# Kernel tuning notes

Hardware: AMD Instinct MI355X
Metric: run time of the kernel (lower is better)

The kernel has to match this reference:

```python
import jax, jax.numpy as jnp
import numpy as np

N, E, D, H, OUT, L, G = 50000, 800000, 128, 128, 128, 5, 512
EMB = L * H  # 640
BN_EPS = 1e-5


def setup_inputs() -> dict:
    key = jax.random.key(0)
    ks = jax.random.split(key, 24)
    s_h = 1.0 / np.sqrt(H)
    s_e = 1.0 / np.sqrt(EMB)
    inp = {
        'x': jax.random.normal(ks[0], (N, D), jnp.float32),
        'edge_index': jax.random.randint(ks[1], (2, E), 0, N, jnp.int32),
        'batch': jnp.sort(jax.random.randint(ks[2], (N,), 0, G, jnp.int32)),
        # per-layer GINConv MLP: Linear(D/H->H), BN(H), ReLU, Linear(H->H). D==H so stackable.
        'conv_W1': jax.random.normal(ks[3], (L, H, H), jnp.float32) * s_h,
        'conv_b1': jnp.zeros((L, H), jnp.float32),
        'conv_g1': jnp.ones((L, H), jnp.float32),
        'conv_be1': jnp.zeros((L, H), jnp.float32),
        'conv_W2': jax.random.normal(ks[4], (L, H, H), jnp.float32) * s_h,
        'conv_b2': jnp.zeros((L, H), jnp.float32),
        'eps': jnp.zeros((L,), jnp.float32),  # train_eps=True, init 0.0
        # outer BatchNorm per layer
        'bn_g': jnp.ones((L, H), jnp.float32),
        'bn_b': jnp.zeros((L, H), jnp.float32),
        # per-layer prediction heads Linear(H -> OUT)
        'pred_W': jax.random.normal(ks[5], (L, H, OUT), jnp.float32) * s_h,
        'pred_b': jnp.zeros((L, OUT), jnp.float32),
        # global_d FF(EMB): 3 stacked Linear(EMB,EMB) + shortcut
        'gW': jax.random.normal(ks[6], (3, EMB, EMB), jnp.float32) * s_e,
        'gb': jnp.zeros((3, EMB), jnp.float32),
        'gsW': jax.random.normal(ks[7], (EMB, EMB), jnp.float32) * s_e,
        'gsb': jnp.zeros((EMB,), jnp.float32),
        # local_d FF(EMB)
        'lW': jax.random.normal(ks[8], (3, EMB, EMB), jnp.float32) * s_e,
        'lb': jnp.zeros((3, EMB), jnp.float32),
        'lsW': jax.random.normal(ks[9], (EMB, EMB), jnp.float32) * s_e,
        'lsb': jnp.zeros((EMB,), jnp.float32),
    }
    return inp


def _bn(h, g, b):
    # BatchNorm1d, training mode: batch stats over node dim (biased var)
    m = jnp.mean(h, axis=0)
    v = jnp.var(h, axis=0)
    return g * (h - m) * jax.lax.rsqrt(v + BN_EPS) + b


def _ff(x, W, b, Ws, bs):
    h = x
    for i in range(3):
        h = jax.nn.relu(h @ W[i] + b[i])
    return h + x @ Ws + bs


def reference(x, edge_index, batch, conv_W1, conv_b1, conv_g1, conv_be1,
              conv_W2, conv_b2, eps, bn_g, bn_b, pred_W, pred_b,
              gW, gb, gsW, gsb, lW, lb, lsW, lsb):
    src, dst = edge_index[0], edge_index[1]
    h = x
    xs = []
    for i in range(L):
        # GINConv: (1+eps)*x_i + sum_{j->i} x_j, then MLP
        agg = jax.ops.segment_sum(h[src], dst, num_segments=N)
        h = (1.0 + eps[i]) * h + agg
        h = _bn(h @ conv_W1[i] + conv_b1[i], conv_g1[i], conv_be1[i])
        h = jax.nn.relu(h)
        h = h @ conv_W2[i] + conv_b2[i]
        h = jax.nn.relu(_bn(h, bn_g[i], bn_b[i]))
        xs.append(h)
    # per-layer graph sum-pool + prediction head (dropout in eval = identity)
    xpool = [jax.ops.segment_sum(xs[i], batch, num_segments=G) @ pred_W[i] + pred_b[i]
             for i in range(L)]
    xcat = jnp.concatenate(xpool, axis=1)            # [G, L*OUT]
    graph_embedding = _ff(xcat, gW, gb, gsW, gsb)     # [G, EMB]
    node_embedding = _ff(jnp.concatenate(xs, axis=1), lW, lb, lsW, lsb)  # [N, EMB]
    return (graph_embedding, node_embedding, xcat)
```

## Files before the change

kernel.cpp:

```cpp
#include <hip/hip_runtime.h>

constexpr int H    = 128;
constexpr int LNUM = 5;
constexpr int NG   = 512;
constexpr int EMB  = 640;
constexpr float BN_EPS = 1e-5f;

typedef __attribute__((ext_vector_type(8))) short bf16x8;
typedef __attribute__((ext_vector_type(4))) float f32x4;

__device__ inline unsigned short f2bf(float f){
  unsigned u = __builtin_bit_cast(unsigned, f);
  u += 0x7FFF + ((u >> 16) & 1);
  return (unsigned short)(u >> 16);
}
__device__ inline float bf2f(unsigned short h){
  unsigned u = ((unsigned)h) << 16;
  return __builtin_bit_cast(float, u);
}

__device__ inline int xcd_swz(int bid, int nwg){
  int q = nwg >> 3, r = nwg & 7;
  int xcd = bid & 7, idx = bid >> 3;
  return (xcd < r ? xcd*(q+1) : r*(q+1) + (xcd-r)*q) + idx;
}

__global__ void k_zerof(float* p, int n){
  int i = blockIdx.x*256 + threadIdx.x;
  if (i < n) p[i] = 0.f;
}
__global__ void k_zeroi(int* p, int n){
  int i = blockIdx.x*256 + threadIdx.x;
  if (i < n) p[i] = 0;
}

__global__ void k_hist(const int* __restrict__ dst, int E, int* deg){
  int e = blockIdx.x*256 + threadIdx.x;
  if (e < E) atomicAdd(&deg[dst[e]], 1);
}

__global__ __launch_bounds__(1024) void k_scan(int* degcur, int* __restrict__ rowptr, int n){
  __shared__ int wsum[16];
  __shared__ int carry;
  int tid = threadIdx.x, wid = tid >> 6, lane = tid & 63;
  if (tid == 0){ carry = 0; rowptr[0] = 0; }
  __syncthreads();
  for (int base = 0; base < n; base += 1024){
    int v = (base + tid < n) ? degcur[base + tid] : 0;
    int s = v;
#pragma unroll
    for (int off = 1; off < 64; off <<= 1){
      int t = __shfl_up(s, off);
      if (lane >= off) s += t;
    }
    if (lane == 63) wsum[wid] = s;
    __syncthreads();
    if (wid == 0 && lane < 16){
      int wv = wsum[lane];
#pragma unroll
      for (int off = 1; off < 16; off <<= 1){
        int t = __shfl_up(wv, off);
        if (lane >= off) wv += t;
      }
      wsum[lane] = wv;
    }
    __syncthreads();
    int incl = s + (wid ? wsum[wid-1] : 0) + carry;
    if (base + tid < n){ rowptr[base + tid + 1] = incl; degcur[base + tid] = incl - v; }
    __syncthreads();
    if (tid == 0) carry += wsum[15];
    __syncthreads();
  }
}

__global__ void k_scatter(const int* __restrict__ src, const int* __restrict__ dst,
                          int E, int* cursor, int* __restrict__ colsrc){
  int e = blockIdx.x*256 + threadIdx.x;
  if (e < E){
    int d = dst[e];
    int pos = atomicAdd(&cursor[d], 1);
    colsrc[pos] = src[e];
  }
}

__global__ void k_gstart(const int* __restrict__ batch, int N, int* __restrict__ gstart){
  int g = blockIdx.x*256 + threadIdx.x;
  if (g <= NG){
    int lo = 0, hi = N;
    while (lo < hi){
      int mid = (lo + hi) >> 1;
      if (batch[mid] < g) lo = mid + 1; else hi = mid;
    }
    gstart[g] = lo;
  }
}

__global__ void k_castT(const float* __restrict__ W, unsigned short* __restrict__ Wt,
                        int K, int Nn, int ldt, int koff){
  __shared__ float sh[32][33];
  const size_t in_off  = (size_t)blockIdx.z * K * Nn;
  const size_t out_off = (size_t)blockIdx.z * Nn * ldt;
  int n0 = blockIdx.x*32, k0 = blockIdx.y*32;
  int tx = threadIdx.x, ty = threadIdx.y;
  for (int r = ty; r < 32; r += 8)
    sh[r][tx] = W[in_off + (size_t)(k0 + r)*Nn + n0 + tx];
  __syncthreads();
  for (int r = ty; r < 32; r += 8)
    Wt[out_off + (size_t)(n0 + r)*ldt + koff + k0 + tx] = f2bf(sh[tx][r]);
}

__global__ void k_bias2(const float* __restrict__ a, const float* __restrict__ b,
                        float* __restrict__ o){
  int i = threadIdx.x;
  o[i] = a[i] + b[i];
}

__global__ __launch_bounds__(320) void k_pool(const unsigned short* __restrict__ xall,
                                              const int* __restrict__ gstart,
                                              float* __restrict__ pooled){
  int g = blockIdx.x;
  int t = threadIdx.x;
  int n0 = gstart[g], n1 = gstart[g+1];
  float a0 = 0.f, a1 = 0.f;
  for (int n = n0; n < n1; ++n){
    unsigned u = ((const unsigned*)xall)[(size_t)n*(EMB/2) + t];
    a0 += bf2f((unsigned short)u); a1 += bf2f((unsigned short)(u >> 16));
  }
  *(float2*)(pooled + (size_t)g*EMB + 2*t) = make_float2(a0, a1);
}

__global__ __launch_bounds__(128) void k_pred(const float* __restrict__ pooled,
                                              const float* __restrict__ W,
                                              const float* __restrict__ b,
                                              float* __restrict__ xcat){
  int g = blockIdx.x, l = blockIdx.y, o = threadIdx.x;
  __shared__ float sh[128];
  sh[o] = pooled[(size_t)g*EMB + l*H + o];
  __syncthreads();
  const float* Wl = W + (size_t)l*H*H;
  float acc = b[l*H + o];
  for (int k = 0; k < H; ++k) acc = fmaf(sh[k], Wl[k*H + o], acc);
  xcat[(size_t)g*EMB + l*H + o] = acc;
}

template<bool RELU, bool OUT_BF16, bool DUAL>
__global__ __launch_bounds__(512) void k_mm(
    const unsigned short* __restrict__ A, int lda,
    const unsigned short* __restrict__ A2,
    const unsigned short* __restrict__ Bt, int ldb,
    const float* __restrict__ bias,
    void* __restrict__ Cv, int ldc,
    int M, int K)
{
  __shared__ union LdsU {
    unsigned short stage[2][2][8192];
    unsigned short sc16[128*136];
    float          sc32[128*132];
  } u;
  const int tid  = threadIdx.x;
  const int lane = tid & 63;
  const int w    = tid >> 6;
  const int wr   = w >> 2, wc = w & 3;

  const int nwg = gridDim.x * gridDim.y;
  const int bid = blockIdx.y * gridDim.x + blockIdx.x;
  const int wg  = xcd_swz(bid, nwg);
  const int col0 = (wg % gridDim.x) * 128;
  const int row0 = (wg / gridDim.x) * 128;
  const int KA   = DUAL ? (K >> 1) : K;

  const unsigned short *sA[2], *sA2p[2], *sB[2];
  int dOff[2];
#pragma unroll
  for (int j = 0; j < 2; ++j){
    int d = w*2048 + j*1024 + lane*16;
    int m = d >> 7;
    int inner = (d & 127) ^ ((m & 7) << 4);
    int gm = row0 + m; if (gm > M-1) gm = M-1;
    sA[j]  = A + (size_t)gm*lda + (inner >> 1);
    if (DUAL) sA2p[j] = A2 + (size_t)gm*lda + (inner >> 1);
    sB[j]  = Bt + (size_t)(col0 + m)*ldb + (inner >> 1);
    dOff[j] = w*2048 + j*1024;
  }

  f32x4 acc[4][2];
#pragma unroll
  for (int i = 0; i < 4; ++i)
#pragma unroll
    for (int j = 0; j < 2; ++j)
      acc[i][j] = (f32x4){0.f, 0.f, 0.f, 0.f};

  auto STAGE = [&](int buf, int kt){
    int k0 = kt*64, ka = k0;
    bool second = DUAL && (k0 >= KA);
    if (second) ka = k0 - KA;
#pragma unroll
    for (int j = 0; j < 2; ++j){
      const unsigned short* s = second ? (sA2p[j] + ka) : (sA[j] + ka);
      __builtin_amdgcn_global_load_lds(
          (const __attribute__((address_space(1))) void*)s,
          (__attribute__((address_space(3))) void*)((char*)&u.stage[buf][0][0] + dOff[j]),
          16, 0, 0);
    }
#pragma unroll
    for (int j = 0; j < 2; ++j)
      __builtin_amdgcn_global_load_lds(
          (const __attribute__((address_space(1))) void*)(sB[j] + k0),
          (__attribute__((address_space(3))) void*)((char*)&u.stage[buf][1][0] + dOff[j]),
          16, 0, 0);
  };

  const int NT = K / 64;
  STAGE(0, 0);
  STAGE(1, 1);
  asm volatile("s_waitcnt vmcnt(4)" ::: "memory");
  asm volatile("s_barrier" ::: "memory");

  for (int t = 0; t < NT; ++t){
    const char* Ab = (const char*)&u.stage[t & 1][0][0];
    const char* Bb = (const char*)&u.stage[t & 1][1][0];
    bf16x8 af[2][4], bq[2][2];
#pragma unroll
    for (int kk = 0; kk < 2; ++kk){
      const int kb = kk*64 + ((lane >> 4) << 4);
#pragma unroll
      for (int i = 0; i < 4; ++i){
        int row = wr*64 + i*16 + (lane & 15);
        af[kk][i] = *(const bf16x8*)(Ab + ((row*128 + kb) ^ ((row & 7) << 4)));
      }
#pragma unroll
      for (int j = 0; j < 2; ++j){
        int col = wc*32 + j*16 + (lane & 15);
        bq[kk][j] = *(const bf16x8*)(Bb + ((col*128 + kb) ^ ((col & 7) << 4)));
      }
    }
    if (t + 2 < NT){
      asm volatile("s_barrier" ::: "memory");
      STAGE(t & 1, t + 2);
    }
#pragma unroll
    for (int kk = 0; kk < 2; ++kk)
#pragma unroll
      for (int i = 0; i < 4; ++i)
#pragma unroll
        for (int j = 0; j < 2; ++j)
          acc[i][j] = __builtin_amdgcn_mfma_f32_16x16x32_bf16(af[kk][i], bq[kk][j], acc[i][j], 0, 0, 0);
    if (t + 1 < NT){
      if (t + 2 < NT) asm volatile("s_waitcnt vmcnt(4)" ::: "memory");
      else            asm volatile("s_waitcnt vmcnt(0)" ::: "memory");
      asm volatile("s_barrier" ::: "memory");
    }
  }

  __syncthreads();
  if (OUT_BF16){
#pragma unroll
    for (int j = 0; j < 2; ++j){
      int cl = wc*32 + j*16 + (lane & 15);
      float bs = bias[col0 + cl];
#pragma unroll
      for (int i = 0; i < 4; ++i){
        int rb = wr*64 + i*16 + ((lane >> 4) << 2);
#pragma unroll
        for (int r = 0; r < 4; ++r){
          float v = acc[i][j][r] + bs;
          if (RELU) v = fmaxf(v, 0.f);
          u.sc16[(rb + r)*136 + cl] = f2bf(v);
        }
      }
    }
    __syncthreads();
    unsigned short* Cb = (unsigned short*)Cv;
    for (int idx = tid; idx < 128*16; idx += 512){
      int rr = idx >> 4, seg = idx & 15;
      int grow = row0 + rr;
      if (grow < M){
        uint4 vv = *(const uint4*)&u.sc16[rr*136 + seg*8];
        *(uint4*)(Cb + (size_t)grow*ldc + col0 + seg*8) = vv;
      }
    }
  } else {
#pragma unroll
    for (int j = 0; j < 2; ++j){
      int cl = wc*32 + j*16 + (lane & 15);
      float bs = bias[col0 + cl];
#pragma unroll
      for (int i = 0; i < 4; ++i){
        int rb = wr*64 + i*16 + ((lane >> 4) << 2);
#pragma unroll
        for (int r = 0; r < 4; ++r){
          float v = acc[i][j][r] + bs;
          if (RELU) v = fmaxf(v, 0.f);
          u.sc32[(rb + r)*132 + cl] = v;
        }
      }
    }
    __syncthreads();
    float* Cf = (float*)Cv;
    for (int idx = tid; idx < 128*32; idx += 512){
      int rr = idx >> 5, seg = idx & 31;
      int grow = row0 + rr;
      if (grow < M){
        float4 vv = *(const float4*)&u.sc32[rr*132 + seg*4];
        *(float4*)(Cf + (size_t)grow*ldc + col0 + seg*4) = vv;
      }
    }
  }
}

template<bool IN_BF16>
__global__ __launch_bounds__(512) void k_mmca(
    const void* __restrict__ hin, int ldh,
    const int* __restrict__ rowptr, const int* __restrict__ colsrc,
    const float* __restrict__ epsp,
    const unsigned short* __restrict__ Bt,
    const float* __restrict__ bias,
    unsigned short* __restrict__ C, int ldc,
    float* __restrict__ sums, float* __restrict__ sumsq,
    int M)
{
  __shared__ unsigned short shm[2*128*128];
  unsigned short* As = shm;
  unsigned short* Bs = shm + 16384;
  const int tid  = threadIdx.x;
  const int lane = tid & 63;
  const int w    = tid >> 6;
  const int wr   = w >> 2, wc = w & 3;

  const int wg   = xcd_swz(blockIdx.x, gridDim.x);
  const int row0 = wg * 128;

#pragma unroll
  for (int j = 0; j < 4; ++j){
    int d = w*4096 + j*1024 + lane*16;
    int m = d >> 8;
    int inner = (d & 255) ^ ((m & 15) << 4);
    __builtin_amdgcn_global_load_lds(
        (const __attribute__((address_space(1))) void*)(Bt + (size_t)m*H + (inner >> 1)),
        (__attribute__((address_space(3))) void*)((char*)Bs + w*4096 + j*1024),
        16, 0, 0);
  }

  {
    int r  = tid >> 2;
    int c0 = (tid & 3) << 5;
    int node = row0 + r; if (node > M-1) node = M-1;
    float ep = 1.0f + *epsp;
    float a[32];
    if (IN_BF16){
      const unsigned short* src = (const unsigned short*)hin + (size_t)node*ldh + c0;
#pragma unroll
      for (int q = 0; q < 4; ++q){
        uint2 v = *(const uint2*)(src + q*8);
        a[q*8+0] = ep*bf2f((unsigned short)v.x);  a[q*8+1] = ep*bf2f((unsigned short)(v.x>>16));
        uint2 v2 = *(const uint2*)(src + q*8 + 4);
        a[q*8+2] = ep*bf2f((unsigned short)v.y);  a[q*8+3] = ep*bf2f((unsigned short)(v.y>>16));
        a[q*8+4] = ep*bf2f((unsigned short)v2.x); a[q*8+5] = ep*bf2f((unsigned short)(v2.x>>16));
        a[q*8+6] = ep*bf2f((unsigned short)v2.y); a[q*8+7] = ep*bf2f((unsigned short)(v2.y>>16));
      }
    } else {
      const float* src = (const float*)hin + (size_t)node*ldh + c0;
#pragma unroll
      for (int q = 0; q < 32; q += 4){
        float4 f = *(const float4*)(src + q);
        a[q] = ep*f.x; a[q+1] = ep*f.y; a[q+2] = ep*f.z; a[q+3] = ep*f.w;
      }
    }
    int e = rowptr[node], e1 = rowptr[node+1];
    for (; e < e1; ++e){
      int s = colsrc[e];
      if (IN_BF16){
        const unsigned short* p = (const unsigned short*)hin + (size_t)s*ldh + c0;
        uint4 v0 = *(const uint4*)(p);
        uint4 v1 = *(const uint4*)(p + 8);
        uint4 v2 = *(const uint4*)(p + 16);
        uint4 v3 = *(const uint4*)(p + 24);
        const unsigned* uu[4] = {(const unsigned*)&v0, (const unsigned*)&v1,
                                 (const unsigned*)&v2, (const unsigned*)&v3};
#pragma unroll
        for (int q = 0; q < 4; ++q)
#pragma unroll
          for (int k = 0; k < 4; ++k){
            unsigned x = uu[q][k];
            a[q*8 + 2*k]     += bf2f((unsigned short)x);
            a[q*8 + 2*k + 1] += bf2f((unsigned short)(x >> 16));
          }
      } else {
        const float* p = (const float*)hin + (size_t)s*ldh + c0;
#pragma unroll
        for (int q = 0; q < 32; q += 4){
          float4 f = *(const float4*)(p + q);
          a[q] += f.x; a[q+1] += f.y; a[q+2] += f.z; a[q+3] += f.w;
        }
      }
    }
#pragma unroll
    for (int q = 0; q < 4; ++q){
      unsigned pk[4];
#pragma unroll
      for (int k = 0; k < 4; ++k)
        pk[k] = (unsigned)f2bf(a[q*8 + 2*k]) | ((unsigned)f2bf(a[q*8 + 2*k + 1]) << 16);
      int byte = (r*256 + (tid & 3)*64 + q*16) ^ ((r & 15) << 4);
      *(uint4*)((char*)As + byte) = *(uint4*)pk;
    }
  }

  asm volatile("s_waitcnt vmcnt(0)" ::: "memory");
  __syncthreads();

  f32x4 acc[4][2];
#pragma unroll
  for (int i = 0; i < 4; ++i)
#pragma unroll
    for (int j = 0; j < 2; ++j)
      acc[i][j] = (f32x4){0.f, 0.f, 0.f, 0.f};

#pragma unroll
  for (int kk = 0; kk < 4; ++kk){
    const int kb = kk*64 + ((lane >> 4) << 4);
    bf16x8 af[4], bfr[2];
#pragma unroll
    for (int i = 0; i < 4; ++i){
      int row = wr*64 + i*16 + (lane & 15);
      af[i] = *(const bf16x8*)((const char*)As + ((row*256 + kb) ^ ((row & 15) << 4)));
    }
#pragma unroll
    for (int j = 0; j < 2; ++j){
      int col = wc*32 + j*16 + (lane & 15);
      bfr[j] = *(const bf16x8*)((const char*)Bs + ((col*256 + kb) ^ ((col & 15) << 4)));
    }
#pragma unroll
    for (int i = 0; i < 4; ++i)
#pragma unroll
      for (int j = 0; j < 2; ++j)
        acc[i][j] = __builtin_amdgcn_mfma_f32_16x16x32_bf16(af[i], bfr[j], acc[i][j], 0, 0, 0);
  }

#pragma unroll
  for (int j = 0; j < 2; ++j){
    int col = wc*32 + j*16 + (lane & 15);
    float bs = bias[col];
    float s = 0.f, q = 0.f;
#pragma unroll
    for (int i = 0; i < 4; ++i){
      int rb = row0 + wr*64 + i*16 + ((lane >> 4) << 2);
#pragma unroll
      for (int r = 0; r < 4; ++r){
        if (rb + r < M){
          float v = acc[i][j][r] + bs;
          s += v; q += v*v;
        }
      }
    }
    s += __shfl_xor(s, 16); q += __shfl_xor(q, 16);
    s += __shfl_xor(s, 32); q += __shfl_xor(q, 32);
    if (lane < 16){
      atomicAdd(&sums[col], s);
      atomicAdd(&sumsq[col], q);
    }
  }

  __syncthreads();
#pragma unroll
  for (int j = 0; j < 2; ++j){
    int cl = wc*32 + j*16 + (lane & 15);
    float bs = bias[cl];
#pragma unroll
    for (int i = 0; i < 4; ++i){
      int rb = wr*64 + i*16 + ((lane >> 4) << 2);
#pragma unroll
      for (int r = 0; r < 4; ++r)
        shm[(rb + r)*136 + cl] = f2bf(acc[i][j][r] + bs);
    }
  }
  __syncthreads();
  for (int idx = tid; idx < 128*16; idx += 512){
    int rr = idx >> 4, seg = idx & 15;
    int grow = row0 + rr;
    if (grow < M){
      uint4 vv = *(const uint4*)&shm[rr*136 + seg*8];
      *(uint4*)(C + (size_t)grow*ldc + seg*8) = vv;
    }
  }
}

__global__ __launch_bounds__(512) void k_mmc2(
    const unsigned short* __restrict__ A,
    const unsigned short* __restrict__ Bt,
    const float* __restrict__ bias,
    const float* __restrict__ statin,
    const float* __restrict__ g1, const float* __restrict__ be1,
    float invn,
    unsigned short* __restrict__ C, int ldc,
    float* __restrict__ sums, float* __restrict__ sumsq,
    int M)
{
  __shared__ unsigned short shm[2*128*128];
  __shared__ float bnsc[128], bnsf[128];
  unsigned short* As = shm;
  unsigned short* Bs = shm + 16384;
  const int tid  = threadIdx.x;
  const int lane = tid & 63;
  const int w    = tid >> 6;
  const int wr   = w >> 2, wc = w & 3;

  const int wg   = xcd_swz(blockIdx.x, gridDim.x);
  const int row0 = wg * 128;

#pragma unroll
  for (int j = 0; j < 4; ++j){
    int d = w*4096 + j*1024 + lane*16;
    int m = d >> 8;
    int inner = (d & 255) ^ ((m & 15) << 4);
    int gm = row0 + m; if (gm > M-1) gm = M-1;
    __builtin_amdgcn_global_load_lds(
        (const __attribute__((address_space(1))) void*)(A + (size_t)gm*H + (inner >> 1)),
        (__attribute__((address_space(3))) void*)((char*)As + w*4096 + j*1024),
        16, 0, 0);
    __builtin_amdgcn_global_load_lds(
        (const __attribute__((address_space(1))) void*)(Bt + (size_t)m*H + (inner >> 1)),
        (__attribute__((address_space(3))) void*)((char*)Bs + w*4096 + j*1024),
        16, 0, 0);
  }

  if (tid < 128){
    float m = statin[tid]*invn;
    float v = statin[128 + tid]*invn - m*m;
    float inv = rsqrtf(v + BN_EPS);
    float sc = g1[tid]*inv;
    bnsc[tid] = sc;
    bnsf[tid] = be1[tid] - m*sc;
  }

  asm volatile("s_waitcnt vmcnt(0)" ::: "memory");
  __syncthreads();

  f32x4 acc[4][2];
#pragma unroll
  for (int i = 0; i < 4; ++i)
#pragma unroll
    for (int j = 0; j < 2; ++j)
      acc[i][j] = (f32x4){0.f, 0.f, 0.f, 0.f};

#pragma unroll
  for (int kk = 0; kk < 4; ++kk){
    const int kb = kk*64 + ((lane >> 4) << 4);
    bf16x8 af[4], bfr[2];
#pragma unroll
    for (int i = 0; i < 4; ++i){
      int row = wr*64 + i*16 + (lane & 15);
      af[i] = *(const bf16x8*)((const char*)As + ((row*256 + kb) ^ ((row & 15) << 4)));
    }
#pragma unroll
    for (int j = 0; j < 2; ++j){
      int col = wc*32 + j*16 + (lane & 15);
      bfr[j] = *(const bf16x8*)((const char*)Bs + ((col*256 + kb) ^ ((col & 15) << 4)));
    }
    {
      int k8 = kk*32 + ((lane >> 4) << 3);
      float4 s0 = *(const float4*)(&bnsc[k8]), s1 = *(const float4*)(&bnsc[k8 + 4]);
      float4 f0 = *(const float4*)(&bnsf[k8]), f1 = *(const float4*)(&bnsf[k8 + 4]);
      float sc[8] = {s0.x,s0.y,s0.z,s0.w,s1.x,s1.y,s1.z,s1.w};
      float sf[8] = {f0.x,f0.y,f0.z,f0.w,f1.x,f1.y,f1.z,f1.w};
#pragma unroll
      for (int i = 0; i < 4; ++i){
        bf16x8 aa = af[i], o;
#pragma unroll
        for (int jj = 0; jj < 8; ++jj){
          float v = fmaxf(fmaf(sc[jj], bf2f((unsigned short)aa[jj]), sf[jj]), 0.f);
          o[jj] = (short)f2bf(v);
        }
        af[i] = o;
      }
    }
#pragma unroll
    for (int i = 0; i < 4; ++i)
#pragma unroll
      for (int j = 0; j < 2; ++j)
        acc[i][j] = __builtin_amdgcn_mfma_f32_16x16x32_bf16(af[i], bfr[j], acc[i][j], 0, 0, 0);
  }

#pragma unroll
  for (int j = 0; j < 2; ++j){
    int col = wc*32 + j*16 + (lane & 15);
    float bs = bias[col];
    float s = 0.f, q = 0.f;
#pragma unroll
    for (int i = 0; i < 4; ++i){
      int rb = row0 + wr*64 + i*16 + ((lane >> 4) << 2);
#pragma unroll
      for (int r = 0; r < 4; ++r){
        if (rb + r < M){
          float v = acc[i][j][r] + bs;
          s += v; q += v*v;
        }
      }
    }
    s += __shfl_xor(s, 16); q += __shfl_xor(q, 16);
    s += __shfl_xor(s, 32); q += __shfl_xor(q, 32);
    if (lane < 16){
      atomicAdd(&sums[col], s);
      atomicAdd(&sumsq[col], q);
    }
  }

  __syncthreads();
#pragma unroll
  for (int j = 0; j < 2; ++j){
    int cl = wc*32 + j*16 + (lane & 15);
    float bs = bias[cl];
#pragma unroll
    for (int i = 0; i < 4; ++i){
      int rb = wr*64 + i*16 + ((lane >> 4) << 2);
#pragma unroll
      for (int r = 0; r < 4; ++r)
        shm[(rb + r)*136 + cl] = f2bf(acc[i][j][r] + bs);
    }
  }
  __syncthreads();
  for (int idx = tid; idx < 128*16; idx += 512){
    int rr = idx >> 4, seg = idx & 15;
    int grow = row0 + rr;
    if (grow < M){
      uint4 vv = *(const uint4*)&shm[rr*136 + seg*8];
      *(uint4*)(C + (size_t)grow*ldc + seg*8) = vv;
    }
  }
}

__global__ __launch_bounds__(256) void k_bnapply(const unsigned short* __restrict__ U,
                                                 const float* __restrict__ statp,
                                                 const float* __restrict__ g,
                                                 const float* __restrict__ b,
                                                 float invn,
                                                 unsigned short* __restrict__ out,
                                                 int ldo, int n){
  int i = blockIdx.x*256 + threadIdx.x;
  int total = n * (H/4);
  if (i < total){
    int r = i >> 5;
    int c4 = (i & 31) << 2;
    float4 sm = *(const float4*)(statp + c4);
    float4 sq = *(const float4*)(statp + 128 + c4);
    float4 gg = *(const float4*)(g + c4);
    float4 bb = *(const float4*)(b + c4);
    float m0 = sm.x*invn, m1 = sm.y*invn, m2 = sm.z*invn, m3 = sm.w*invn;
    float s0 = gg.x*rsqrtf(sq.x*invn - m0*m0 + BN_EPS);
    float s1 = gg.y*rsqrtf(sq.y*invn - m1*m1 + BN_EPS);
    float s2 = gg.z*rsqrtf(sq.z*invn - m2*m2 + BN_EPS);
    float s3 = gg.w*rsqrtf(sq.w*invn - m3*m3 + BN_EPS);
    float f0 = bb.x - m0*s0, f1 = bb.y - m1*s1, f2 = bb.z - m2*s2, f3 = bb.w - m3*s3;
    uint2 up = *(const uint2*)(U + (size_t)r*H + c4);
    float a = fmaxf(fmaf(s0, bf2f((unsigned short)up.x),       f0), 0.f);
    float c = fmaxf(fmaf(s1, bf2f((unsigned short)(up.x>>16)), f1), 0.f);
    float d = fmaxf(fmaf(s2, bf2f((unsigned short)up.y),       f2), 0.f);
    float e = fmaxf(fmaf(s3, bf2f((unsigned short)(up.y>>16)), f3), 0.f);
    uint2 o;
    o.x = (unsigned)f2bf(a) | ((unsigned)f2bf(c) << 16);
    o.y = (unsigned)f2bf(d) | ((unsigned)f2bf(e) << 16);
    *(uint2*)(out + (size_t)r*ldo + c4) = o;
  }
}

template<bool RELU, bool ADD_D>
__global__ __launch_bounds__(256) void k_gemm64(
    const float* __restrict__ A, int lda,
    const float* __restrict__ B, int ldb,
    const float* __restrict__ bias,
    const float* D, int ldd,
    float* C, int ldc,
    int M, int N, int K)
{
  __shared__ float As[32][68];
  __shared__ float Bs[32][64];
  const int tid  = threadIdx.x;
  const int tx   = tid & 15;
  const int ty   = tid >> 4;
  const int row0 = blockIdx.x * 64;
  const int col0 = blockIdx.y * 64;
  const int am = tid >> 3;
  const int ak = (tid & 7) << 2;
  const int bk = tid >> 4;
  const int bn = (tid & 15) << 2;
  float acc[4][4] = {};

  for (int k0 = 0; k0 < K; k0 += 32){
#pragma unroll
    for (int h = 0; h < 2; ++h){
      int m  = am + h*32;
      int gr = row0 + m;
      float4 v = make_float4(0.f, 0.f, 0.f, 0.f);
      if (gr < M) v = *(const float4*)(A + (size_t)gr*lda + k0 + ak);
      As[ak+0][m]=v.x; As[ak+1][m]=v.y; As[ak+2][m]=v.z; As[ak+3][m]=v.w;
    }
#pragma unroll
    for (int h = 0; h < 2; ++h){
      int kk = bk + h*16;
      *(float4*)(&Bs[kk][bn]) = *(const float4*)(B + (size_t)(k0+kk)*ldb + col0 + bn);
    }
    __syncthreads();
#pragma unroll 8
    for (int k = 0; k < 32; ++k){
      float4 a = *(const float4*)(&As[k][ty<<2]);
      float4 b = *(const float4*)(&Bs[k][tx<<2]);
      float av[4] = {a.x,a.y,a.z,a.w};
      float bv[4] = {b.x,b.y,b.z,b.w};
#pragma unroll
      for (int i = 0; i < 4; ++i)
#pragma unroll
        for (int j = 0; j < 4; ++j)
          acc[i][j] = fmaf(av[i], bv[j], acc[i][j]);
    }
    __syncthreads();
  }

  const int col = col0 + (tx<<2);
  float4 bv = *(const float4*)(bias + col);
#pragma unroll
  for (int i = 0; i < 4; ++i){
    int row = row0 + (ty<<2) + i;
    if (row < M){
      float r[4] = {acc[i][0]+bv.x, acc[i][1]+bv.y, acc[i][2]+bv.z, acc[i][3]+bv.w};
      if (RELU){
#pragma unroll
        for (int j = 0; j < 4; ++j) r[j] = fmaxf(r[j], 0.f);
      }
      if (ADD_D){
        float4 d = *(const float4*)(D + (size_t)row*ldd + col);
        r[0]+=d.x; r[1]+=d.y; r[2]+=d.z; r[3]+=d.w;
      }
      *(float4*)(C + (size_t)row*ldc + col) = make_float4(r[0],r[1],r[2],r[3]);
    }
  }
}

extern "C" void kernel_launch(void* const* d_in, const int* in_sizes, int n_in,
                              void* d_out, int out_size, void* d_ws, size_t ws_size,
                              hipStream_t stream) {
  const float* x        = (const float*)d_in[0];
  const int*   ei       = (const int*)d_in[1];
  const int*   batch    = (const int*)d_in[2];
  const float* conv_W1  = (const float*)d_in[3];
  const float* conv_b1  = (const float*)d_in[4];
  const float* conv_g1  = (const float*)d_in[5];
  const float* conv_be1 = (const float*)d_in[6];
  const float* conv_W2  = (const float*)d_in[7];
  const float* conv_b2  = (const float*)d_in[8];
  const float* epsv     = (const float*)d_in[9];
  const float* bn_g     = (const float*)d_in[10];
  const float* bn_b     = (const float*)d_in[11];
  const float* pred_W   = (const float*)d_in[12];
  const float* pred_b   = (const float*)d_in[13];
  const float* gW       = (const float*)d_in[14];
  const float* gb       = (const float*)d_in[15];
  const float* gsW      = (const float*)d_in[16];
  const float* gsb      = (const float*)d_in[17];
  const float* lW       = (const float*)d_in[18];
  const float* lb       = (const float*)d_in[19];
  const float* lsW      = (const float*)d_in[20];
  const float* lsb      = (const float*)d_in[21];

  const int N = in_sizes[0] / H;
  const int E = in_sizes[1] / 2;
  const int* srcI = ei;
  const int* dstI = ei + E;

  float* out = (float*)d_out;
  float* GE = out;
  float* NE = out + (size_t)NG*EMB;
  float* XC = NE + (size_t)N*EMB;

  unsigned short* xall = (unsigned short*)d_ws;
  unsigned short* h1   = xall + (size_t)N*EMB;
  unsigned short* h2   = h1 + (size_t)N*EMB;
  unsigned short* ub   = h1;
  unsigned short* tb   = h1 + (size_t)N*H;

  float* pooled  = (float*)(h2 + (size_t)N*EMB);
  float* gtmp1   = pooled + (size_t)NG*EMB;
  float* gtmp2   = gtmp1 + (size_t)NG*EMB;
  float* slots   = gtmp2 + (size_t)NG*EMB;
  float* biasNE  = slots + 2560;
  unsigned short* W1t   = (unsigned short*)(biasNE + EMB);
  unsigned short* W2t   = W1t + (size_t)LNUM*H*H;
  unsigned short* lWt01 = W2t + (size_t)LNUM*H*H;
  unsigned short* Wcat  = lWt01 + (size_t)2*EMB*EMB;
  int* rowptr = (int*)(Wcat + (size_t)2*EMB*EMB);
  int* cursor = rowptr + (N + 1);
  int* colsrc = cursor + N;
  int* gstart = colsrc + E;

  k_zerof<<<10, 256, 0, stream>>>(slots, 2560);

  k_zeroi<<<(N+255)/256, 256, 0, stream>>>(cursor, N);
  k_hist<<<(E+255)/256, 256, 0, stream>>>(dstI, E, cursor);
  k_scan<<<1, 1024, 0, stream>>>(cursor, rowptr, N);
  k_scatter<<<(E+255)/256, 256, 0, stream>>>(srcI, dstI, E, cursor, colsrc);
  k_gstart<<<(NG+256)/256, 256, 0, stream>>>(batch, N, gstart);

  const dim3 tb32(32, 8);
  k_castT<<<dim3(H/32, H/32, LNUM), tb32, 0, stream>>>(conv_W1, W1t, H, H, H, 0);
  k_castT<<<dim3(H/32, H/32, LNUM), tb32, 0, stream>>>(conv_W2, W2t, H, H, H, 0);
  k_castT<<<dim3(EMB/32, EMB/32, 2), tb32, 0, stream>>>(lW, lWt01, EMB, EMB, EMB, 0);
  k_castT<<<dim3(EMB/32, EMB/32, 1), tb32, 0, stream>>>(lW + (size_t)2*EMB*EMB, Wcat,
                                                        EMB, EMB, 2*EMB, 0);
  k_castT<<<dim3(EMB/32, EMB/32, 1), tb32, 0, stream>>>(lsW, Wcat, EMB, EMB, 2*EMB, EMB);
  k_bias2<<<1, EMB, 0, stream>>>(lb + (size_t)2*EMB, lsb, biasNE);

  const float invn = 1.0f / (float)N;
  const int nrow = (N + 127)/128;

  for (int l = 0; l < LNUM; ++l){
    float* slot1 = slots + (size_t)l*512;
    float* slot2 = slot1 + 256;

    if (l == 0)
      k_mmca<false><<<nrow, 512, 0, stream>>>(
          x, H, rowptr, colsrc, epsv, W1t, conv_b1,
          ub, H, slot1, slot1 + 128, N);
    else
      k_mmca<true><<<nrow, 512, 0, stream>>>(
          xall + (size_t)(l-1)*H, EMB, rowptr, colsrc, epsv + l,
          W1t + (size_t)l*H*H, conv_b1 + l*H,
          ub, H, slot1, slot1 + 128, N);

    k_mmc2<<<nrow, 512, 0, stream>>>(
        ub, W2t + (size_t)l*H*H, conv_b2 + l*H,
        slot1, conv_g1 + l*H, conv_be1 + l*H, invn,
        tb, H, slot2, slot2 + 128, N);

    k_bnapply<<<(N*32 + 255)/256, 256, 0, stream>>>(
        tb, slot2, bn_g + l*H, bn_b + l*H, invn,
        xall + (size_t)l*H, EMB, N);
  }

  k_pool<<<NG, 320, 0, stream>>>(xall, gstart, pooled);
  k_pred<<<dim3(NG, LNUM), 128, 0, stream>>>(pooled, pred_W, pred_b, XC);

  const dim3 gg((NG + 63)/64, EMB/64);
  k_gemm64<false,false><<<gg, 256, 0, stream>>>(XC, EMB, gsW, EMB, gsb,
                                                nullptr, 0, GE, EMB, NG, EMB, EMB);
  k_gemm64<true,false><<<gg, 256, 0, stream>>>(XC, EMB, gW, EMB, gb,
                                               nullptr, 0, gtmp1, EMB, NG, EMB, EMB);
  k_gemm64<true,false><<<gg, 256, 0, stream>>>(gtmp1, EMB, gW + (size_t)EMB*EMB, EMB, gb + EMB,
                                               nullptr, 0, gtmp2, EMB, NG, EMB, EMB);
  k_gemm64<true,true><<<gg, 256, 0, stream>>>(gtmp2, EMB, gW + (size_t)2*EMB*EMB, EMB, gb + 2*EMB,
                                              GE, EMB, GE, EMB, NG, EMB, EMB);

  const dim3 gn(EMB/128, nrow);
  k_mm<true,true,false><<<gn, 512, 0, stream>>>(
      xall, EMB, nullptr, lWt01, EMB, lb, h1, EMB, N, EMB);
  k_mm<true,true,false><<<gn, 512, 0, stream>>>(
      h1, EMB, nullptr, lWt01 + (size_t)EMB*EMB, EMB, lb + EMB, h2, EMB, N, EMB);
  k_mm<false,false,true><<<gn, 512, 0, stream>>>(
      h2, EMB, xall, Wcat, 2*EMB, biasNE, NE, EMB, N, 2*EMB);
}
```

Before: 1.074 ms.

## Replace BN atomics with per-block partials, warp-per-row gather, sorted CSR, smaller FF tiles

The batch-norm statistics are now written as per-workgroup partial sums and reduced later, which removes the global float atomics and the zeroing kernel. Neighbor aggregation gives each row to one wavefront that reads 128-channel rows in a coalesced way, two edges at a time. CSR segments are sorted by source for locality, graph pooling applies BN+ReLU from the pre-BN buffer, and the small graph FF GEMM uses 32-row tiles for more blocks. The cost is an extra insertion-sort kernel, a reduction over roughly 391 partials in every consuming block, and a serial per-wave edge loop.

```diff
diff --git a/kernel.cpp b/kernel.cpp
--- a/kernel.cpp
+++ b/kernel.cpp
@@ -25,10 +25,6 @@
   return (xcd < r ? xcd*(q+1) : r*(q+1) + (xcd-r)*q) + idx;
 }
 
-__global__ void k_zerof(float* p, int n){
-  int i = blockIdx.x*256 + threadIdx.x;
-  if (i < n) p[i] = 0.f;
-}
 __global__ void k_zeroi(int* p, int n){
   int i = blockIdx.x*256 + threadIdx.x;
   if (i < n) p[i] = 0;
@@ -80,6 +76,19 @@
     int d = dst[e];
     int pos = atomicAdd(&cursor[d], 1);
     colsrc[pos] = src[e];
+  }
+}
+
+__global__ void k_sortseg(const int* __restrict__ rowptr, int* __restrict__ colsrc, int n){
+  int node = blockIdx.x*256 + threadIdx.x;
+  if (node < n){
+    int lo = rowptr[node], hi = rowptr[node+1];
+    for (int i = lo + 1; i < hi; ++i){
+      int v = colsrc[i];
+      int j = i - 1;
+      while (j >= lo && colsrc[j] > v){ colsrc[j+1] = colsrc[j]; --j; }
+      colsrc[j+1] = v;
+    }
   }
 }
 
@@ -115,16 +124,23 @@
   o[i] = a[i] + b[i];
 }
 
-__global__ __launch_bounds__(320) void k_pool(const unsigned short* __restrict__ xall,
+__global__ __launch_bounds__(320) void k_pool(const unsigned short* __restrict__ xpre,
+                                              const float* __restrict__ bnsc2,
+                                              const float* __restrict__ bnsf2,
                                               const int* __restrict__ gstart,
                                               float* __restrict__ pooled){
   int g = blockIdx.x;
   int t = threadIdx.x;
+  int f0 = 2*t;
+  int l = f0 >> 7, c = f0 & 127;
+  float sc0 = bnsc2[l*128 + c],     sf0 = bnsf2[l*128 + c];
+  float sc1 = bnsc2[l*128 + c + 1], sf1 = bnsf2[l*128 + c + 1];
   int n0 = gstart[g], n1 = gstart[g+1];
   float a0 = 0.f, a1 = 0.f;
   for (int n = n0; n < n1; ++n){
-    unsigned u = ((const unsigned*)xall)[(size_t)n*(EMB/2) + t];
-    a0 += bf2f((unsigned short)u); a1 += bf2f((unsigned short)(u >> 16));
+    unsigned u = ((const unsigned*)xpre)[(size_t)n*(EMB/2) + t];
+    a0 += fmaxf(fmaf(sc0, bf2f((unsigned short)u),        sf0), 0.f);
+    a1 += fmaxf(fmaf(sc1, bf2f((unsigned short)(u >> 16)), sf1), 0.f);
   }
   *(float2*)(pooled + (size_t)g*EMB + 2*t) = make_float2(a0, a1);
 }
@@ -316,10 +332,11 @@
     const unsigned short* __restrict__ Bt,
     const float* __restrict__ bias,
     unsigned short* __restrict__ C, int ldc,
-    float* __restrict__ sums, float* __restrict__ sumsq,
+    float* __restrict__ pa,
     int M)
 {
   __shared__ unsigned short shm[2*128*128];
+  __shared__ float sbs[2][128], sbq[2][128];
   unsigned short* As = shm;
   unsigned short* Bs = shm + 16384;
   const int tid  = threadIdx.x;
@@ -342,66 +359,46 @@
   }
 
   {
-    int r  = tid >> 2;
-    int c0 = (tid & 3) << 5;
-    int node = row0 + r; if (node > M-1) node = M-1;
+    const int ld2 = ldh >> 1;
     float ep = 1.0f + *epsp;
-    float a[32];
-    if (IN_BF16){
-      const unsigned short* src = (const unsigned short*)hin + (size_t)node*ldh + c0;
-#pragma unroll
-      for (int q = 0; q < 4; ++q){
-        uint2 v = *(const uint2*)(src + q*8);
-        a[q*8+0] = ep*bf2f((unsigned short)v.x);  a[q*8+1] = ep*bf2f((unsigned short)(v.x>>16));
-        uint2 v2 = *(const uint2*)(src + q*8 + 4);
-        a[q*8+2] = ep*bf2f((unsigned short)v.y);  a[q*8+3] = ep*bf2f((unsigned short)(v.y>>16));
-        a[q*8+4] = ep*bf2f((unsigned short)v2.x); a[q*8+5] = ep*bf2f((unsigned short)(v2.x>>16));
-        a[q*8+6] = ep*bf2f((unsigned short)v2.y); a[q*8+7] = ep*bf2f((unsigned short)(v2.y>>16));
-      }
-    } else {
-      const float* src = (const float*)hin + (size_t)node*ldh + c0;
-#pragma unroll
-      for (int q = 0; q < 32; q += 4){
-        float4 f = *(const float4*)(src + q);
-        a[q] = ep*f.x; a[q+1] = ep*f.y; a[q+2] = ep*f.z; a[q+3] = ep*f.w;
-      }
-    }
-    int e = rowptr[node], e1 = rowptr[node+1];
-    for (; e < e1; ++e){
-      int s = colsrc[e];
+    for (int rr = 0; rr < 16; ++rr){
+      int r = w*16 + rr;
+      int node = row0 + r; if (node > M-1) node = M-1;
+      float a0, a1;
       if (IN_BF16){
-        const unsigned short* p = (const unsigned short*)hin + (size_t)s*ldh + c0;
-        uint4 v0 = *(const uint4*)(p);
-        uint4 v1 = *(const uint4*)(p + 8);
-        uint4 v2 = *(const uint4*)(p + 16);
-        uint4 v3 = *(const uint4*)(p + 24);
-        const unsigned* uu[4] = {(const unsigned*)&v0, (const unsigned*)&v1,
-                                 (const unsigned*)&v2, (const unsigned*)&v3};
-#pragma unroll
-        for (int q = 0; q < 4; ++q)
-#pragma unroll
-          for (int k = 0; k < 4; ++k){
-            unsigned x = uu[q][k];
-            a[q*8 + 2*k]     += bf2f((unsigned short)x);
-            a[q*8 + 2*k + 1] += bf2f((unsigned short)(x >> 16));
-          }
+        unsigned v = ((const unsigned*)hin)[(size_t)node*ld2 + lane];
+        a0 = ep*bf2f((unsigned short)v); a1 = ep*bf2f((unsigned short)(v >> 16));
       } else {
-        const float* p = (const float*)hin + (size_t)s*ldh + c0;
-#pragma unroll
-        for (int q = 0; q < 32; q += 4){
-          float4 f = *(const float4*)(p + q);
-          a[q] += f.x; a[q+1] += f.y; a[q+2] += f.z; a[q+3] += f.w;
+        float2 f = ((const float2*)hin)[(size_t)node*ld2 + lane];
+        a0 = ep*f.x; a1 = ep*f.y;
+      }
+      int e = rowptr[node], e1 = rowptr[node+1];
+      for (; e + 2 <= e1; e += 2){
+        int s0 = colsrc[e], s1 = colsrc[e+1];
+        if (IN_BF16){
+          unsigned v0 = ((const unsigned*)hin)[(size_t)s0*ld2 + lane];
+          unsigned v1 = ((const unsigned*)hin)[(size_t)s1*ld2 + lane];
+          a0 += bf2f((unsigned short)v0) + bf2f((unsigned short)v1);
+          a1 += bf2f((unsigned short)(v0 >> 16)) + bf2f((unsigned short)(v1 >> 16));
+        } else {
+          float2 f0 = ((const float2*)hin)[(size_t)s0*ld2 + lane];
+          float2 f1 = ((const float2*)hin)[(size_t)s1*ld2 + lane];
+          a0 += f0.x + f1.x; a1 += f0.y + f1.y;
         }
       }
-    }
-#pragma unroll
-    for (int q = 0; q < 4; ++q){
-      unsigned pk[4];
-#pragma unroll
-      for (int k = 0; k < 4; ++k)
-        pk[k] = (unsigned)f2bf(a[q*8 + 2*k]) | ((unsigned)f2bf(a[q*8 + 2*k + 1]) << 16);
-      int byte = (r*256 + (tid & 3)*64 + q*16) ^ ((r & 15) << 4);
-      *(uint4*)((char*)As + byte) = *(uint4*)pk;
+      for (; e < e1; ++e){
+        int s = colsrc[e];
+        if (IN_BF16){
+          unsigned v = ((const unsigned*)hin)[(size_t)s*ld2 + lane];
+          a0 += bf2f((unsigned short)v); a1 += bf2f((unsigned short)(v >> 16));
+        } else {
+          float2 f = ((const float2*)hin)[(size_t)s*ld2 + lane];
+          a0 += f.x; a1 += f.y;
+        }
+      }
+      unsigned pk = (unsigned)f2bf(a0) | ((unsigned)f2bf(a1) << 16);
+      int byte = (r*256 + lane*4) ^ ((r & 15) << 4);
+      *(unsigned*)((char*)As + byte) = pk;
     }
   }
 
@@ -454,10 +451,12 @@
     }
     s += __shfl_xor(s, 16); q += __shfl_xor(q, 16);
     s += __shfl_xor(s, 32); q += __shfl_xor(q, 32);
-    if (lane < 16){
-      atomicAdd(&sums[col], s);
-      atomicAdd(&sumsq[col], q);
-    }
+    if (lane < 16){ sbs[wr][col] = s; sbq[wr][col] = q; }
+  }
+  __syncthreads();
+  if (tid < 128){
+    pa[(size_t)wg*256 + tid]       = sbs[0][tid] + sbs[1][tid];
+    pa[(size_t)wg*256 + 128 + tid] = sbq[0][tid] + sbq[1][tid];
   }
 
   __syncthreads();
@@ -488,23 +487,25 @@
     const unsigned short* __restrict__ A,
     const unsigned short* __restrict__ Bt,
     const float* __restrict__ bias,
-    const float* __restrict__ statin,
+    const float* __restrict__ pa,
     const float* __restrict__ g1, const float* __restrict__ be1,
     float invn,
     unsigned short* __restrict__ C, int ldc,
-    float* __restrict__ sums, float* __restrict__ sumsq,
+    float* __restrict__ pb,
     int M)
 {
   __shared__ unsigned short shm[2*128*128];
   __shared__ float bnsc[128], bnsf[128];
+  __shared__ float rs[4][128], rq[4][128];
   unsigned short* As = shm;
   unsigned short* Bs = shm + 16384;
   const int tid  = threadIdx.x;
   const int lane = tid & 63;
   const int w    = tid >> 6;
   const int wr   = w >> 2, wc = w & 3;
-
-  const int wg   = xcd_swz(blockIdx.x, gridDim.x);
+  const int nwg  = gridDim.x;
+
+  const int wg   = xcd_swz(blockIdx.x, nwg);
   const int row0 = wg * 128;
 
 #pragma unroll
@@ -523,9 +524,21 @@
         16, 0, 0);
   }
 
+  {
+    int c = tid & 127, part = tid >> 7;
+    float s = 0.f, q = 0.f;
+    for (int bi = part; bi < nwg; bi += 4){
+      s += pa[(size_t)bi*256 + c];
+      q += pa[(size_t)bi*256 + 128 + c];
+    }
+    rs[part][c] = s; rq[part][c] = q;
+  }
+  __syncthreads();
   if (tid < 128){
-    float m = statin[tid]*invn;
-    float v = statin[128 + tid]*invn - m*m;
+    float s = rs[0][tid] + rs[1][tid] + rs[2][tid] + rs[3][tid];
+    float q = rq[0][tid] + rq[1][tid] + rq[2][tid] + rq[3][tid];
+    float m = s*invn;
+    float v = q*invn - m*m;
     float inv = rsqrtf(v + BN_EPS);
     float sc = g1[tid]*inv;
     bnsc[tid] = sc;
@@ -580,6 +593,7 @@
         acc[i][j] = __builtin_amdgcn_mfma_f32_16x16x32_bf16(af[i], bfr[j], acc[i][j], 0, 0, 0);
   }
 
+  __syncthreads();
 #pragma unroll
   for (int j = 0; j < 2; ++j){
     int col = wc*32 + j*16 + (lane & 15);
@@ -598,10 +612,12 @@
     }
     s += __shfl_xor(s, 16); q += __shfl_xor(q, 16);
     s += __shfl_xor(s, 32); q += __shfl_xor(q, 32);
-    if (lane < 16){
-      atomicAdd(&sums[col], s);
-      atomicAdd(&sumsq[col], q);
-    }
+    if (lane < 16){ rs[wr][col] = s; rq[wr][col] = q; }
+  }
+  __syncthreads();
+  if (tid < 128){
+    pb[(size_t)wg*256 + tid]       = rs[0][tid] + rs[1][tid];
+    pb[(size_t)wg*256 + 128 + tid] = rq[0][tid] + rq[1][tid];
   }
 
   __syncthreads();
@@ -628,11 +644,38 @@
   }
 }
 
+__global__ __launch_bounds__(512) void k_bnfin2(const float* __restrict__ pb,
+                                                const float* __restrict__ g,
+                                                const float* __restrict__ b,
+                                                float* __restrict__ scale,
+                                                float* __restrict__ shift,
+                                                float invn, int nwg){
+  __shared__ float rs[4][128], rq[4][128];
+  int tid = threadIdx.x;
+  int c = tid & 127, part = tid >> 7;
+  float s = 0.f, q = 0.f;
+  for (int bi = part; bi < nwg; bi += 4){
+    s += pb[(size_t)bi*256 + c];
+    q += pb[(size_t)bi*256 + 128 + c];
+  }
+  rs[part][c] = s; rq[part][c] = q;
+  __syncthreads();
+  if (tid < 128){
+    float S = rs[0][tid] + rs[1][tid] + rs[2][tid] + rs[3][tid];
+    float Q = rq[0][tid] + rq[1][tid] + rq[2][tid] + rq[3][tid];
+    float m = S*invn;
+    float v = Q*invn - m*m;
+    float inv = rsqrtf(v + BN_EPS);
+    float sc = g[tid]*inv;
+    scale[tid] = sc;
+    shift[tid] = b[tid] - m*sc;
+  }
+}
+
 __global__ __launch_bounds__(256) void k_bnapply(const unsigned short* __restrict__ U,
-                                                 const float* __restrict__ statp,
-                                                 const float* __restrict__ g,
-                                                 const float* __restrict__ b,
-                                                 float invn,
+                                                 int ldu,
+                                                 const float* __restrict__ scale,
+                                                 const float* __restrict__ shift,
                                                  unsigned short* __restrict__ out,
                                                  int ldo, int n){
   int i = blockIdx.x*256 + threadIdx.x;
@@ -640,21 +683,13 @@
   if (i < total){
     int r = i >> 5;
     int c4 = (i & 31) << 2;
-    float4 sm = *(const float4*)(statp + c4);
-    float4 sq = *(const float4*)(statp + 128 + c4);
-    float4 gg = *(const float4*)(g + c4);
-    float4 bb = *(const float4*)(b + c4);
-    float m0 = sm.x*invn, m1 = sm.y*invn, m2 = sm.z*invn, m3 = sm.w*invn;
-    float s0 = gg.x*rsqrtf(sq.x*invn - m0*m0 + BN_EPS);
-    float s1 = gg.y*rsqrtf(sq.y*invn - m1*m1 + BN_EPS);
-    float s2 = gg.z*rsqrtf(sq.z*invn - m2*m2 + BN_EPS);
-    float s3 = gg.w*rsqrtf(sq.w*invn - m3*m3 + BN_EPS);
-    float f0 = bb.x - m0*s0, f1 = bb.y - m1*s1, f2 = bb.z - m2*s2, f3 = bb.w - m3*s3;
-    uint2 up = *(const uint2*)(U + (size_t)r*H + c4);
-    float a = fmaxf(fmaf(s0, bf2f((unsigned short)up.x),       f0), 0.f);
-    float c = fmaxf(fmaf(s1, bf2f((unsigned short)(up.x>>16)), f1), 0.f);
-    float d = fmaxf(fmaf(s2, bf2f((unsigned short)up.y),       f2), 0.f);
-    float e = fmaxf(fmaf(s3, bf2f((unsigned short)(up.y>>16)), f3), 0.f);
+    uint2 up = *(const uint2*)(U + (size_t)r*ldu + c4);
+    float4 sc = *(const float4*)(scale + c4);
+    float4 sf = *(const float4*)(shift + c4);
+    float a = fmaxf(fmaf(sc.x, bf2f((unsigned short)up.x),       sf.x), 0.f);
+    float c = fmaxf(fmaf(sc.y, bf2f((unsigned short)(up.x>>16)), sf.y), 0.f);
+    float d = fmaxf(fmaf(sc.z, bf2f((unsigned short)up.y),       sf.z), 0.f);
+    float e = fmaxf(fmaf(sc.w, bf2f((unsigned short)(up.y>>16)), sf.w), 0.f);
     uint2 o;
     o.x = (unsigned)f2bf(a) | ((unsigned)f2bf(c) << 16);
     o.y = (unsigned)f2bf(d) | ((unsigned)f2bf(e) << 16);
@@ -671,27 +706,25 @@
     float* C, int ldc,
     int M, int N, int K)
 {
-  __shared__ float As[32][68];
+  __shared__ float As[32][36];
   __shared__ float Bs[32][64];
   const int tid  = threadIdx.x;
   const int tx   = tid & 15;
   const int ty   = tid >> 4;
-  const int row0 = blockIdx.x * 64;
+  const int row0 = blockIdx.x * 32;
   const int col0 = blockIdx.y * 64;
   const int am = tid >> 3;
   const int ak = (tid & 7) << 2;
   const int bk = tid >> 4;
   const int bn = (tid & 15) << 2;
-  float acc[4][4] = {};
+  float acc[2][4] = {};
 
   for (int k0 = 0; k0 < K; k0 += 32){
-#pragma unroll
-    for (int h = 0; h < 2; ++h){
-      int m  = am + h*32;
-      int gr = row0 + m;
+    {
+      int gr = row0 + am;
       float4 v = make_float4(0.f, 0.f, 0.f, 0.f);
       if (gr < M) v = *(const float4*)(A + (size_t)gr*lda + k0 + ak);
-      As[ak+0][m]=v.x; As[ak+1][m]=v.y; As[ak+2][m]=v.z; As[ak+3][m]=v.w;
+      As[ak+0][am]=v.x; As[ak+1][am]=v.y; As[ak+2][am]=v.z; As[ak+3][am]=v.w;
     }
 #pragma unroll
     for (int h = 0; h < 2; ++h){
@@ -701,12 +734,12 @@
     __syncthreads();
 #pragma unroll 8
     for (int k = 0; k < 32; ++k){
-      float4 a = *(const float4*)(&As[k][ty<<2]);
+      float2 a = *(const float2*)(&As[k][ty<<1]);
       float4 b = *(const float4*)(&Bs[k][tx<<2]);
-      float av[4] = {a.x,a.y,a.z,a.w};
-      float bv[4] = {b.x,b.y,b.z,b.w};
-#pragma unroll
-      for (int i = 0; i < 4; ++i)
+      float av[2] = {a.x, a.y};
+      float bv[4] = {b.x, b.y, b.z, b.w};
+#pragma unroll
+      for (int i = 0; i < 2; ++i)
 #pragma unroll
         for (int j = 0; j < 4; ++j)
           acc[i][j] = fmaf(av[i], bv[j], acc[i][j]);
@@ -717,8 +750,8 @@
   const int col = col0 + (tx<<2);
   float4 bv = *(const float4*)(bias + col);
 #pragma unroll
-  for (int i = 0; i < 4; ++i){
-    int row = row0 + (ty<<2) + i;
+  for (int i = 0; i < 2; ++i){
+    int row = row0 + (ty<<1) + i;
     if (row < M){
       float r[4] = {acc[i][0]+bv.x, acc[i][1]+bv.y, acc[i][2]+bv.z, acc[i][3]+bv.w};
       if (RELU){
@@ -774,13 +807,17 @@
   unsigned short* h1   = xall + (size_t)N*EMB;
   unsigned short* h2   = h1 + (size_t)N*EMB;
   unsigned short* ub   = h1;
-  unsigned short* tb   = h1 + (size_t)N*H;
+  unsigned short* xpre = h2;
 
   float* pooled  = (float*)(h2 + (size_t)N*EMB);
   float* gtmp1   = pooled + (size_t)NG*EMB;
   float* gtmp2   = gtmp1 + (size_t)NG*EMB;
-  float* slots   = gtmp2 + (size_t)NG*EMB;
-  float* biasNE  = slots + 2560;
+  const int nrow = (N + 127)/128;
+  float* pa      = gtmp2 + (size_t)NG*EMB;
+  float* pb      = pa + (size_t)nrow*256;
+  float* bnsc2   = pb + (size_t)nrow*256;
+  float* bnsf2   = bnsc2 + LNUM*128;
+  float* biasNE  = bnsf2 + LNUM*128;
   unsigned short* W1t   = (unsigned short*)(biasNE + EMB);
   unsigned short* W2t   = W1t + (size_t)LNUM*H*H;
   unsigned short* lWt01 = W2t + (size_t)LNUM*H*H;
@@ -790,12 +827,11 @@
   int* colsrc = cursor + N;
   int* gstart = colsrc + E;
 
-  k_zerof<<<10, 256, 0, stream>>>(slots, 2560);
-
   k_zeroi<<<(N+255)/256, 256, 0, stream>>>(cursor, N);
   k_hist<<<(E+255)/256, 256, 0, stream>>>(dstI, E, cursor);
   k_scan<<<1, 1024, 0, stream>>>(cursor, rowptr, N);
   k_scatter<<<(E+255)/256, 256, 0, stream>>>(srcI, dstI, E, cursor, colsrc);
+  k_sortseg<<<(N+255)/256, 256, 0, stream>>>(rowptr, colsrc, N);
   k_gstart<<<(NG+256)/256, 256, 0, stream>>>(batch, N, gstart);
 
   const dim3 tb32(32, 8);
@@ -808,36 +844,33 @@
   k_bias2<<<1, EMB, 0, stream>>>(lb + (size_t)2*EMB, lsb, biasNE);
 
   const float invn = 1.0f / (float)N;
-  const int nrow = (N + 127)/128;
 
   for (int l = 0; l < LNUM; ++l){
-    float* slot1 = slots + (size_t)l*512;
-    float* slot2 = slot1 + 256;
-
     if (l == 0)
       k_mmca<false><<<nrow, 512, 0, stream>>>(
-          x, H, rowptr, colsrc, epsv, W1t, conv_b1,
-          ub, H, slot1, slot1 + 128, N);
+          x, H, rowptr, colsrc, epsv, W1t, conv_b1, ub, H, pa, N);
     else
       k_mmca<true><<<nrow, 512, 0, stream>>>(
           xall + (size_t)(l-1)*H, EMB, rowptr, colsrc, epsv + l,
-          W1t + (size_t)l*H*H, conv_b1 + l*H,
-          ub, H, slot1, slot1 + 128, N);
+          W1t + (size_t)l*H*H, conv_b1 + l*H, ub, H, pa, N);
 
     k_mmc2<<<nrow, 512, 0, stream>>>(
         ub, W2t + (size_t)l*H*H, conv_b2 + l*H,
-        slot1, conv_g1 + l*H, conv_be1 + l*H, invn,
-        tb, H, slot2, slot2 + 128, N);
+        pa, conv_g1 + l*H, conv_be1 + l*H, invn,
+        xpre + (size_t)l*H, EMB, pb, N);
+
+    k_bnfin2<<<1, 512, 0, stream>>>(pb, bn_g + l*H, bn_b + l*H,
+                                    bnsc2 + l*128, bnsf2 + l*128, invn, nrow);
 
     k_bnapply<<<(N*32 + 255)/256, 256, 0, stream>>>(
-        tb, slot2, bn_g + l*H, bn_b + l*H, invn,
+        xpre + (size_t)l*H, EMB, bnsc2 + l*128, bnsf2 + l*128,
         xall + (size_t)l*H, EMB, N);
   }
 
-  k_pool<<<NG, 320, 0, stream>>>(xall, gstart, pooled);
+  k_pool<<<NG, 320, 0, stream>>>(xpre, bnsc2, bnsf2, gstart, pooled);
   k_pred<<<dim3(NG, LNUM), 128, 0, stream>>>(pooled, pred_W, pred_b, XC);
 
-  const dim3 gg((NG + 63)/64, EMB/64);
+  const dim3 gg((NG + 31)/32, EMB/64);
   k_gemm64<false,false><<<gg, 256, 0, stream>>>(XC, EMB, gsW, EMB, gsb,
                                                 nullptr, 0, GE, EMB, NG, EMB, EMB);
   k_gemm64<true,false><<<gg, 256, 0, stream>>>(XC, EMB, gW, EMB, gb,
```

New measurement: 1.512 ms. +40.8%, slower.
